# Kernel optimization log

Hardware: AMD Instinct MI355X
Metric: run time of the kernel (lower is better)

Reference implementation:

```python
import math
import jax, jax.numpy as jnp
import numpy as np

B, H, W, C = 16, 64, 64, 256


def setup_inputs() -> dict:
    key = jax.random.key(0)
    ks = jax.random.split(key, 6)
    return {
        "h": jax.random.normal(ks[0], (B, H, W, C), jnp.float32),
        # grouped 3x3 perception conv: groups=C, in/groups=1, out=3C
        "w_perc": jax.random.normal(ks[1], (3 * C, 1, 3, 3), jnp.float32) * 0.1,
        "b_perc": jnp.zeros((3 * C,), jnp.float32),
        # update_net: 1x1 conv 3C->2C, GELU, 1x1 conv 2C->C
        "w_up1": jax.random.normal(ks[2], (2 * C, 3 * C, 1, 1), jnp.float32) * 0.02,
        "b_up1": jnp.zeros((2 * C,), jnp.float32),
        "w_up2": jax.random.normal(ks[3], (C, 2 * C, 1, 1), jnp.float32) * 0.02,
        "b_up2": jnp.zeros((C,), jnp.float32),
        # lin_qkv: Linear C -> 3C (torch weight layout [out,in])
        "w_qkv": jax.random.normal(ks[4], (3 * C, C), jnp.float32) * 0.02,
        "b_qkv": jnp.zeros((3 * C,), jnp.float32),
    }


_POS = [(-1, -1), (-1, 0), (-1, 1), (0, -1), (0, 0), (0, 1), (1, -1), (1, 0), (1, 1)]


def _local_attn(hn, w_qkv, b_qkv):
    """3x3 windowed local attention (zero-padded borders), NHWC in/out."""
    Bb, Hh, Ww, Cc = hn.shape
    qkv = jnp.einsum('bhwc,dc->bhwd', hn, w_qkv) + b_qkv
    q, k, v = jnp.split(qkv, 3, axis=-1)
    kp = jnp.pad(k, ((0, 0), (1, 1), (1, 1), (0, 0)))
    vp = jnp.pad(v, ((0, 0), (1, 1), (1, 1), (0, 0)))
    scale = 1.0 / math.sqrt(Cc)
    # scores over the 9 neighbor offsets -> [B,H,W,9]
    scores = jnp.stack(
        [(q * kp[:, 1 + dy:1 + dy + Hh, 1 + dx:1 + dx + Ww, :]).sum(-1) for dy, dx in _POS],
        axis=-1) * scale
    w = jax.nn.softmax(scores, axis=-1)
    out = jnp.zeros_like(v)
    for i, (dy, dx) in enumerate(_POS):
        out = out + w[..., i:i + 1] * vp[:, 1 + dy:1 + dy + Hh, 1 + dx:1 + dx + Ww, :]
    return out


def reference(h, w_perc, b_perc, w_up1, b_up1, w_up2, b_up2, w_qkv, b_qkv):
    # eval-mode forward: noise / dropout / stochastic mask are identity
    Cc = h.shape[-1]
    x = jnp.transpose(h, (0, 3, 1, 2))  # NCHW
    perceived = jax.lax.conv_general_dilated(
        x, w_perc, window_strides=(1, 1), padding='SAME',
        feature_group_count=Cc,
        dimension_numbers=('NCHW', 'OIHW', 'NCHW')) + b_perc[None, :, None, None]
    hid = jnp.einsum('bphw,dp->bdhw', perceived, w_up1[:, :, 0, 0]) + b_up1[None, :, None, None]
    hid = jax.nn.gelu(hid, approximate=False)
    dx = jnp.einsum('bdhw,cd->bchw', hid, w_up2[:, :, 0, 0]) + b_up2[None, :, None, None]
    x_new = x + dx  # stochastic_update in eval mode
    h_new = jnp.transpose(x_new, (0, 2, 3, 1))  # NHWC
    h_attn = _local_attn(h_new, w_qkv, b_qkv)
    return h_new + h_attn
```

## Files before the change

kernel.cpp:

```cpp
#include <hip/hip_runtime.h>
#include <math.h>


typedef unsigned short u16;
typedef __bf16 bf16x8 __attribute__((ext_vector_type(8)));
typedef float floatx4 __attribute__((ext_vector_type(4)));

__device__ int g_flag;
__device__ __align__(16) u16 g_h[16777216];
__device__ __align__(16) u16 g_perc[50331648];
__device__ __align__(16) u16 g_hnew[16777216];
__device__ __align__(16) u16 g_wperc[6912];
__device__ __align__(16) u16 g_bperc[768];
__device__ __align__(16) u16 g_wup1[393216];
__device__ __align__(16) u16 g_bup1[512];
__device__ __align__(16) u16 g_wup2[131072];
__device__ __align__(16) u16 g_bup2[256];
__device__ __align__(16) u16 g_wqkv[196608];
__device__ __align__(16) u16 g_bqkv[768];

__device__ __forceinline__ float b2f(u16 x) {
  unsigned int u = ((unsigned int)x) << 16;
  float f;
  __builtin_memcpy(&f, &u, 4);
  return f;
}
__device__ __forceinline__ u16 f2b(float f) {
  unsigned int u;
  __builtin_memcpy(&u, &f, 4);
  u += 0x7FFFu + ((u >> 16) & 1u);
  return (u16)(u >> 16);
}
__device__ __forceinline__ void gload16(const u16* g, u16* l) {
  __builtin_amdgcn_global_load_lds(
      (const __attribute__((address_space(1))) unsigned int*)g,
      (__attribute__((address_space(3))) unsigned int*)l, 16, 0, 0);
}
__device__ __forceinline__ void up8(const uint4& v, float* f) {
  f[0] = b2f((u16)(v.x & 0xFFFF)); f[1] = b2f((u16)(v.x >> 16));
  f[2] = b2f((u16)(v.y & 0xFFFF)); f[3] = b2f((u16)(v.y >> 16));
  f[4] = b2f((u16)(v.z & 0xFFFF)); f[5] = b2f((u16)(v.z >> 16));
  f[6] = b2f((u16)(v.w & 0xFFFF)); f[7] = b2f((u16)(v.w >> 16));
}
__device__ __forceinline__ void ld8(const u16* p, float* f) {
  uint4 v = *(const uint4*)p;
  up8(v, f);
}

__global__ __launch_bounds__(256) void probe_kernel(const u16* __restrict__ h) {
  __shared__ int hit;
  if (threadIdx.x == 0) hit = 0;
  __syncthreads();
  int local = 0;
  for (int i = threadIdx.x; i < 8192; i += 256) {
    u16 v = h[2 * i];
    if ((v & 0x7F80) == 0x7F80) local = 1;
  }
  if (local) atomicOr(&hit, 1);
  __syncthreads();
  if (threadIdx.x == 0) g_flag = hit;
}

__global__ __launch_bounds__(256) void conv_w_kernel(
    const void* i1, const void* i2, const void* i3, const void* i4,
    const void* i5, const void* i6, const void* i7, const void* i8) {
  const void* srcs[8] = {i1, i2, i3, i4, i5, i6, i7, i8};
  u16* dsts[8] = {g_wperc, g_bperc, g_wup1, g_bup1,
                  g_wup2,  g_bup2,  g_wqkv, g_bqkv};
  const int szs[8] = {6912, 768, 393216, 512, 131072, 256, 196608, 768};
  const int fp32 = g_flag;
  const int stride = gridDim.x * 256;
  for (int gw = blockIdx.x * 256 + threadIdx.x; gw < 730112; gw += stride) {
    int seg = 0, off = gw;
    while (off >= szs[seg]) { off -= szs[seg]; ++seg; }
    dsts[seg][off] = fp32 ? f2b(((const float*)srcs[seg])[off])
                          : ((const u16*)srcs[seg])[off];
  }
}

__global__ __launch_bounds__(256) void perc_kernel(const void* __restrict__ hin) {
  __shared__ __align__(16) u16 sw[3456];
  __shared__ __align__(16) u16 sb[384];
  const int lb = (blockIdx.x & 7) * 256 + (blockIdx.x >> 3);
  const int bid = lb >> 1;
  const int chalf = lb & 1;
  const int b = bid >> 6, y = bid & 63;
  const int xi = threadIdx.x >> 6;
  const int cl = threadIdx.x & 63;
  const int c0 = chalf * 128 + cl * 2;
  for (int i = threadIdx.x; i < 3456; i += 256) sw[i] = g_wperc[chalf * 3456 + i];
  for (int i = threadIdx.x; i < 384; i += 256) sb[i] = g_bperc[chalf * 384 + i];
  const int fp32 = g_flag;
  __syncthreads();
  float w[2][27], bias[2][3];
#pragma unroll
  for (int ch = 0; ch < 2; ++ch) {
    const int lc = cl * 2 + ch;
#pragma unroll
    for (int t = 0; t < 3; ++t) {
      bias[ch][t] = b2f(sb[3 * lc + t]);
#pragma unroll
      for (int j = 0; j < 9; ++j)
        w[ch][t * 9 + j] = b2f(sw[(3 * lc + t) * 9 + j]);
    }
  }
  float hv[3][3][2];
  auto loadcol = [&](int xx, int cc) {
#pragma unroll
    for (int r = 0; r < 3; ++r) {
      const int yy = y - 1 + r;
      const bool ok = ((unsigned)yy < 64u) && ((unsigned)xx < 64u);
      if (ok) {
        const size_t idx = (((size_t)(b * 64 + yy) * 64) + xx) * 256 + c0;
        if (fp32) {
          const float2 v = *(const float2*)((const float*)hin + idx);
          hv[r][cc][0] = v.x;
          hv[r][cc][1] = v.y;
        } else {
          const unsigned v = *(const unsigned*)((const u16*)hin + idx);
          hv[r][cc][0] = b2f((u16)(v & 0xFFFF));
          hv[r][cc][1] = b2f((u16)(v >> 16));
        }
      } else {
        hv[r][cc][0] = 0.0f;
        hv[r][cc][1] = 0.0f;
      }
    }
  };
  const int x0 = xi * 16;
  loadcol(x0 - 1, 0);
  loadcol(x0, 1);
#pragma unroll
  for (int k = 0; k < 16; ++k) {
    const int x = x0 + k;
    loadcol(x + 1, (k + 2) % 3);
    const int cL = k % 3, cM = (k + 1) % 3, cR = (k + 2) % 3;
    const size_t pix = (size_t)(b * 64 + y) * 64 + x;
    *(unsigned*)&g_h[pix * 256 + c0] =
        (unsigned)f2b(hv[1][cM][0]) | ((unsigned)f2b(hv[1][cM][1]) << 16);
    u16* op = &g_perc[pix * 768 + 3 * c0];
    unsigned pk[3];
#pragma unroll
    for (int ch = 0; ch < 2; ++ch) {
#pragma unroll
      for (int t = 0; t < 3; ++t) {
        const float* wt = &w[ch][t * 9];
        float a = bias[ch][t];
        a += hv[0][cL][ch] * wt[0] + hv[0][cM][ch] * wt[1] + hv[0][cR][ch] * wt[2];
        a += hv[1][cL][ch] * wt[3] + hv[1][cM][ch] * wt[4] + hv[1][cR][ch] * wt[5];
        a += hv[2][cL][ch] * wt[6] + hv[2][cM][ch] * wt[7] + hv[2][cR][ch] * wt[8];
        const int o = 3 * ch + t;
        const unsigned bb = f2b(a);
        if (o & 1) pk[o >> 1] |= bb << 16; else pk[o >> 1] = bb;
      }
    }
    *(unsigned*)(op) = pk[0];
    *(unsigned*)(op + 2) = pk[1];
    *(unsigned*)(op + 4) = pk[2];
  }
}

__global__ __launch_bounds__(512, 2) void fused_mlp_qkv() {
  __shared__ __align__(16) u16 L[81920];
  const int tid = threadIdx.x;
  const int w = tid >> 6, lane = tid & 63;
  const int ln = lane & 15, quad = lane >> 4, lnx = ln & 7;
  const int wmi = w >> 2, wni = w & 3;
  const int m_blk = (blockIdx.x & 7) * 64 + (blockIdx.x >> 3);
  const int m0 = m_blk * 128;

  auto stageA = [&](int t) {
    u16* dst = &L[(t & 1) * 8192];
#pragma unroll
    for (int ld = 0; ld < 2; ++ld) {
      const int s = ld * 512 + tid;
      const int sr = s >> 3, sc = (s & 7) ^ (sr & 7);
      gload16(&g_perc[(size_t)(m0 + sr) * 768 + t * 64 + sc * 8], dst + s * 8);
    }
  };
  auto stageB1 = [&](int t) {
    u16* dst = &L[16384 + (t & 1) * 32768];
#pragma unroll
    for (int ld = 0; ld < 8; ++ld) {
      const int s = ld * 512 + tid;
      const int sr = s >> 3, sc = (s & 7) ^ (sr & 7);
      gload16(&g_wup1[(size_t)sr * 768 + t * 64 + sc * 8], dst + s * 8);
    }
  };

  floatx4 acc[4][8] = {};
  stageA(0); stageB1(0);
  for (int u = 0; u < 12; ++u) {
    asm volatile("s_waitcnt vmcnt(0)" ::: "memory");
    __builtin_amdgcn_s_barrier();
    if (u + 1 < 12) { stageA(u + 1); stageB1(u + 1); }
    const u16* Ab = &L[(u & 1) * 8192];
    const u16* Bb = &L[16384 + (u & 1) * 32768];
    bf16x8 a[4][2];
#pragma unroll
    for (int i = 0; i < 4; ++i) {
      const int row = wmi * 64 + i * 16 + ln;
#pragma unroll
      for (int ks = 0; ks < 2; ++ks)
        a[i][ks] = *(const bf16x8*)(Ab + (row * 8 + ((ks * 4 + quad) ^ lnx)) * 8);
    }
    __builtin_amdgcn_s_setprio(1);
#pragma unroll
    for (int jg = 0; jg < 2; ++jg) {
      bf16x8 b[4][2];
#pragma unroll
      for (int jj = 0; jj < 4; ++jj) {
        const int row = wni * 128 + (jg * 4 + jj) * 16 + ln;
#pragma unroll
        for (int ks = 0; ks < 2; ++ks)
          b[jj][ks] =
              *(const bf16x8*)(Bb + (row * 8 + ((ks * 4 + quad) ^ lnx)) * 8);
      }
#pragma unroll
      for (int i = 0; i < 4; ++i)
#pragma unroll
        for (int jj = 0; jj < 4; ++jj)
#pragma unroll
          for (int ks = 0; ks < 2; ++ks)
            acc[i][jg * 4 + jj] = __builtin_amdgcn_mfma_f32_16x16x32_bf16(
                a[i][ks], b[jj][ks], acc[i][jg * 4 + jj], 0, 0, 0);
    }
    __builtin_amdgcn_s_setprio(0);
  }
  __builtin_amdgcn_s_barrier();
#pragma unroll
  for (int i = 0; i < 4; ++i) {
#pragma unroll
    for (int j = 0; j < 8; ++j) {
      const int n = wni * 128 + j * 16 + ln;
      const float bv = b2f(g_bup1[n]);
      const int ch = n >> 3;
#pragma unroll
      for (int rr = 0; rr < 4; ++rr) {
        const int r = wmi * 64 + i * 16 + quad * 4 + rr;
        float v = acc[i][j][rr] + bv;
        v = 0.5f * v * (1.0f + erff(v * 0.70710678118654752f));
        L[((size_t)r * 64 + ((ch & 56) | ((ch & 7) ^ (r & 7)))) * 8 + (n & 7)] =
            f2b(v);
      }
    }
  }
  asm volatile("s_waitcnt lgkmcnt(0)" ::: "memory");
  __builtin_amdgcn_s_barrier();

  auto stageW2 = [&](int t) {
    u16* dst = &L[65536 + (t & 1) * 8192];
#pragma unroll
    for (int ld = 0; ld < 2; ++ld) {
      const int s = ld * 512 + tid;
      const int sr = s >> 2, sc = (s & 3) ^ (sr & 3);
      gload16(&g_wup2[(size_t)sr * 512 + t * 32 + sc * 8], dst + s * 8);
    }
  };
  floatx4 acB[4][4] = {};
  stageW2(0);
  for (int t = 0; t < 16; ++t) {
    asm volatile("s_waitcnt vmcnt(0)" ::: "memory");
    __builtin_amdgcn_s_barrier();
    if (t + 1 < 16) stageW2(t + 1);
    const u16* Wb = &L[65536 + (t & 1) * 8192];
    const int kt = t >> 1, ks = t & 1;
    bf16x8 a[4], b[4];
#pragma unroll
    for (int i = 0; i < 4; ++i) {
      const int row = wmi * 64 + i * 16 + ln;
      a[i] = *(const bf16x8*)(
          &L[((size_t)row * 64 + kt * 8 + ((ks * 4 + quad) ^ (row & 7))) * 8]);
    }
#pragma unroll
    for (int j = 0; j < 4; ++j) {
      const int row = wni * 64 + j * 16 + ln;
      b[j] = *(const bf16x8*)(Wb + (row * 4 + (quad ^ (row & 3))) * 8);
    }
    __builtin_amdgcn_s_setprio(1);
#pragma unroll
    for (int i = 0; i < 4; ++i)
#pragma unroll
      for (int j = 0; j < 4; ++j)
        acB[i][j] = __builtin_amdgcn_mfma_f32_16x16x32_bf16(a[i], b[j],
                                                            acB[i][j], 0, 0, 0);
    __builtin_amdgcn_s_setprio(0);
  }
  __builtin_amdgcn_s_barrier();
#pragma unroll
  for (int i = 0; i < 4; ++i) {
#pragma unroll
    for (int j = 0; j < 4; ++j) {
      const int n = wni * 64 + j * 16 + ln;
      const float bv = b2f(g_bup2[n]);
      const int ch = n >> 3;
#pragma unroll
      for (int rr = 0; rr < 4; ++rr) {
        const int r = wmi * 64 + i * 16 + quad * 4 + rr;
        float v = acB[i][j][rr] + bv;
        v += b2f(g_h[(size_t)(m0 + r) * 256 + n]);
        const u16 bb = f2b(v);
        g_hnew[(size_t)(m0 + r) * 256 + n] = bb;
        L[((size_t)r * 32 + ((ch & 24) | ((ch & 7) ^ (r & 7)))) * 8 + (n & 7)] =
            bb;
      }
    }
  }
  auto stageWq = [&](int tt) {
    u16* dst = &L[32768 + (tt % 3) * 16384];
    const int c = tt >> 2, t = tt & 3;
#pragma unroll
    for (int ld = 0; ld < 4; ++ld) {
      const int s = ld * 512 + tid;
      const int sr = s >> 3, sc = (s & 7) ^ (sr & 7);
      gload16(&g_wqkv[(size_t)(c * 256 + sr) * 256 + t * 64 + sc * 8],
              dst + s * 8);
    }
  };
  stageWq(0);
  stageWq(1);
  asm volatile("s_waitcnt lgkmcnt(0)" ::: "memory");
  __builtin_amdgcn_s_barrier();
  for (int c = 0; c < 3; ++c) {
    floatx4 acC[4][4] = {};
    for (int t = 0; t < 4; ++t) {
      const int tt = c * 4 + t;
      if (tt < 11) asm volatile("s_waitcnt vmcnt(4)" ::: "memory");
      else         asm volatile("s_waitcnt vmcnt(0)" ::: "memory");
      __builtin_amdgcn_s_barrier();
      if (tt + 2 < 12) stageWq(tt + 2);
      const u16* Wb = &L[32768 + (tt % 3) * 16384];
      bf16x8 a[4][2], b[4][2];
#pragma unroll
      for (int i = 0; i < 4; ++i) {
        const int row = wmi * 64 + i * 16 + ln;
#pragma unroll
        for (int ks = 0; ks < 2; ++ks)
          a[i][ks] = *(const bf16x8*)(
              &L[((size_t)row * 32 + t * 8 + ((ks * 4 + quad) ^ (row & 7))) *
                 8]);
      }
#pragma unroll
      for (int j = 0; j < 4; ++j) {
        const int row = wni * 64 + j * 16 + ln;
#pragma unroll
        for (int ks = 0; ks < 2; ++ks)
          b[j][ks] =
              *(const bf16x8*)(Wb + (row * 8 + ((ks * 4 + quad) ^ lnx)) * 8);
      }
      __builtin_amdgcn_s_setprio(1);
#pragma unroll
      for (int i = 0; i < 4; ++i)
#pragma unroll
        for (int j = 0; j < 4; ++j)
#pragma unroll
          for (int ks = 0; ks < 2; ++ks)
            acC[i][j] = __builtin_amdgcn_mfma_f32_16x16x32_bf16(
                a[i][ks], b[j][ks], acC[i][j], 0, 0, 0);
      __builtin_amdgcn_s_setprio(0);
    }
#pragma unroll
    for (int i = 0; i < 4; ++i) {
#pragma unroll
      for (int j = 0; j < 4; ++j) {
        const int n = wni * 64 + j * 16 + ln;
        const float bv = b2f(g_bqkv[c * 256 + n]);
#pragma unroll
        for (int rr = 0; rr < 4; ++rr) {
          const int r = wmi * 64 + i * 16 + quad * 4 + rr;
          g_perc[(size_t)(m0 + r) * 768 + c * 256 + n] = f2b(acC[i][j][rr] + bv);
        }
      }
    }
  }
}

__global__ __launch_bounds__(256) void attn_kernel(void* __restrict__ outv) {
  const int wv = threadIdx.x >> 6, lane = threadIdx.x & 63;
  const int half = lane >> 5, cl = lane & 31;
  const int c0 = cl * 8;
  const int lb = (blockIdx.x & 7) * 128 + (blockIdx.x >> 3);
  const int run = lb * 8 + wv * 2 + half;
  const int row = run >> 3;
  const int y = row & 63;
  const int x0 = (run & 7) * 8;
  const int fp32 = g_flag;

  uint4 Kw[3][3], Vw[3][3], tK[3], tV[3];
  auto fetch = [&](int xx, uint4 (&K3)[3], uint4 (&V3)[3]) {
#pragma unroll
    for (int r = 0; r < 3; ++r) {
      const int yy = y - 1 + r;
      if (((unsigned)yy < 64u) && ((unsigned)xx < 64u)) {
        const size_t np = (size_t)(row - 1 + r) * 64 + xx;
        K3[r] = *(const uint4*)(g_perc + np * 768 + 256 + c0);
        V3[r] = *(const uint4*)(g_perc + np * 768 + 512 + c0);
      } else {
        K3[r] = make_uint4(0, 0, 0, 0);
        V3[r] = make_uint4(0, 0, 0, 0);
      }
    }
  };
  fetch(x0 - 1, tK, tV);
#pragma unroll
  for (int r = 0; r < 3; ++r) { Kw[r][0] = tK[r]; Vw[r][0] = tV[r]; }
  fetch(x0, tK, tV);
#pragma unroll
  for (int r = 0; r < 3; ++r) { Kw[r][1] = tK[r]; Vw[r][1] = tV[r]; }
  fetch(x0 + 1, tK, tV);

#pragma unroll
  for (int k = 0; k < 8; ++k) {
    const int x = x0 + k;
    const int sR = (k + 2) % 3;
#pragma unroll
    for (int r = 0; r < 3; ++r) { Kw[r][sR] = tK[r]; Vw[r][sR] = tV[r]; }
    fetch(x + 2, tK, tV);

    const size_t pix = (size_t)row * 64 + x;
    float q[8];
    ld8(g_perc + pix * 768 + c0, q);
    float a[8];
    ld8(g_hnew + pix * 256 + c0, a);

    float s[9];
#pragma unroll
    for (int j = 0; j < 9; ++j) {
      float kv[8];
      up8(Kw[j / 3][(k + j % 3) % 3], kv);
      float p = q[0] * kv[0] + q[1] * kv[1] + q[2] * kv[2] + q[3] * kv[3] +
                q[4] * kv[4] + q[5] * kv[5] + q[6] * kv[6] + q[7] * kv[7];
#pragma unroll
      for (int off = 16; off >= 1; off >>= 1) p += __shfl_xor(p, off, 64);
      s[j] = p * 0.0625f;
    }
    float mx = s[0];
#pragma unroll
    for (int j = 1; j < 9; ++j) mx = fmaxf(mx, s[j]);
    float e[9], den = 0.0f;
#pragma unroll
    for (int j = 0; j < 9; ++j) {
      e[j] = expf(s[j] - mx);
      den += e[j];
    }
    const float inv = 1.0f / den;
#pragma unroll
    for (int j = 0; j < 9; ++j) {
      const float wgt = e[j] * inv;
      float vv[8];
      up8(Vw[j / 3][(k + j % 3) % 3], vv);
#pragma unroll
      for (int t = 0; t < 8; ++t) a[t] += wgt * vv[t];
    }
    const size_t o = pix * 256 + c0;
    if (fp32) {
      float4 r0 = {a[0], a[1], a[2], a[3]};
      float4 r1 = {a[4], a[5], a[6], a[7]};
      *(float4*)((float*)outv + o) = r0;
      *(float4*)((float*)outv + o + 4) = r1;
    } else {
      uint4 r;
      r.x = (unsigned)f2b(a[0]) | ((unsigned)f2b(a[1]) << 16);
      r.y = (unsigned)f2b(a[2]) | ((unsigned)f2b(a[3]) << 16);
      r.z = (unsigned)f2b(a[4]) | ((unsigned)f2b(a[5]) << 16);
      r.w = (unsigned)f2b(a[6]) | ((unsigned)f2b(a[7]) << 16);
      *(uint4*)((u16*)outv + o) = r;
    }
  }
}

extern "C" void kernel_launch(void* const* d_in, const int* in_sizes, int n_in,
                              void* d_out, int d_out_size, void* d_ws,
                              size_t ws_size, hipStream_t stream) {
  (void)d_ws; (void)ws_size;
  probe_kernel<<<1, 256, 0, stream>>>((const u16*)d_in[0]);
  conv_w_kernel<<<360, 256, 0, stream>>>(d_in[1], d_in[2], d_in[3], d_in[4],
                                         d_in[5], d_in[6], d_in[7], d_in[8]);
  perc_kernel<<<2048, 256, 0, stream>>>(d_in[0]);
  fused_mlp_qkv<<<512, 512, 0, stream>>>();
  attn_kernel<<<1024, 256, 0, stream>>>(d_out);
}
```

Before: 381.6 us.

## Deepen first GEMM pipeline to four stages with smaller K tiles and new swizzle

The first GEMM of the fused MLP kernel drops from a double-buffered 64-wide K tile to a quad-buffered 32-wide K tile with three tiles in flight. It uses partial vmcnt waits so the global loads of later stages overlap with the MFMA work on the current one. The LDS swizzle changes to an XOR on (row>>1)&3, also applied to the W2 staging, to reduce bank conflicts for 4-chunk rows. The cost is twice as many barriers per K, with less MFMA work between them, and the hand-counted vmcnt values have to match the number of loads issued per stage.

```diff
diff --git a/kernel.cpp b/kernel.cpp
--- a/kernel.cpp
+++ b/kernel.cpp
@@ -169,61 +169,54 @@
   const int m_blk = (blockIdx.x & 7) * 64 + (blockIdx.x >> 3);
   const int m0 = m_blk * 128;
 
-  auto stageA = [&](int t) {
-    u16* dst = &L[(t & 1) * 8192];
-#pragma unroll
-    for (int ld = 0; ld < 2; ++ld) {
+  auto stageAW = [&](int t) {
+    u16* base = &L[(t & 3) * 20480];
+    {
+      const int s = tid;
+      const int sr = s >> 2, sc = (s & 3) ^ ((sr >> 1) & 3);
+      gload16(&g_perc[(size_t)(m0 + sr) * 768 + t * 32 + sc * 8], base + s * 8);
+    }
+    u16* wb = base + 4096;
+#pragma unroll
+    for (int ld = 0; ld < 4; ++ld) {
       const int s = ld * 512 + tid;
-      const int sr = s >> 3, sc = (s & 7) ^ (sr & 7);
-      gload16(&g_perc[(size_t)(m0 + sr) * 768 + t * 64 + sc * 8], dst + s * 8);
+      const int sr = s >> 2, sc = (s & 3) ^ ((sr >> 1) & 3);
+      gload16(&g_wup1[(size_t)sr * 768 + t * 32 + sc * 8], wb + s * 8);
     }
   };
-  auto stageB1 = [&](int t) {
-    u16* dst = &L[16384 + (t & 1) * 32768];
-#pragma unroll
-    for (int ld = 0; ld < 8; ++ld) {
-      const int s = ld * 512 + tid;
-      const int sr = s >> 3, sc = (s & 7) ^ (sr & 7);
-      gload16(&g_wup1[(size_t)sr * 768 + t * 64 + sc * 8], dst + s * 8);
-    }
-  };
 
   floatx4 acc[4][8] = {};
-  stageA(0); stageB1(0);
-  for (int u = 0; u < 12; ++u) {
-    asm volatile("s_waitcnt vmcnt(0)" ::: "memory");
+  stageAW(0); stageAW(1); stageAW(2);
+  for (int u = 0; u < 24; ++u) {
+    if (u < 22)       asm volatile("s_waitcnt vmcnt(10)" ::: "memory");
+    else if (u == 22) asm volatile("s_waitcnt vmcnt(5)" ::: "memory");
+    else              asm volatile("s_waitcnt vmcnt(0)" ::: "memory");
     __builtin_amdgcn_s_barrier();
-    if (u + 1 < 12) { stageA(u + 1); stageB1(u + 1); }
-    const u16* Ab = &L[(u & 1) * 8192];
-    const u16* Bb = &L[16384 + (u & 1) * 32768];
-    bf16x8 a[4][2];
+    if (u + 3 < 24) stageAW(u + 3);
+    const u16* Ab = &L[(u & 3) * 20480];
+    const u16* Bb = Ab + 4096;
+    bf16x8 a[4];
 #pragma unroll
     for (int i = 0; i < 4; ++i) {
       const int row = wmi * 64 + i * 16 + ln;
-#pragma unroll
-      for (int ks = 0; ks < 2; ++ks)
-        a[i][ks] = *(const bf16x8*)(Ab + (row * 8 + ((ks * 4 + quad) ^ lnx)) * 8);
+      a[i] = *(const bf16x8*)(Ab + (row * 4 + (quad ^ ((row >> 1) & 3))) * 8);
     }
     __builtin_amdgcn_s_setprio(1);
 #pragma unroll
     for (int jg = 0; jg < 2; ++jg) {
-      bf16x8 b[4][2];
+      bf16x8 b[4];
 #pragma unroll
       for (int jj = 0; jj < 4; ++jj) {
         const int row = wni * 128 + (jg * 4 + jj) * 16 + ln;
-#pragma unroll
-        for (int ks = 0; ks < 2; ++ks)
-          b[jj][ks] =
-              *(const bf16x8*)(Bb + (row * 8 + ((ks * 4 + quad) ^ lnx)) * 8);
+        b[jj] =
+            *(const bf16x8*)(Bb + (row * 4 + (quad ^ ((row >> 1) & 3))) * 8);
       }
 #pragma unroll
       for (int i = 0; i < 4; ++i)
 #pragma unroll
         for (int jj = 0; jj < 4; ++jj)
-#pragma unroll
-          for (int ks = 0; ks < 2; ++ks)
-            acc[i][jg * 4 + jj] = __builtin_amdgcn_mfma_f32_16x16x32_bf16(
-                a[i][ks], b[jj][ks], acc[i][jg * 4 + jj], 0, 0, 0);
+          acc[i][jg * 4 + jj] = __builtin_amdgcn_mfma_f32_16x16x32_bf16(
+              a[i], b[jj], acc[i][jg * 4 + jj], 0, 0, 0);
     }
     __builtin_amdgcn_s_setprio(0);
   }
@@ -253,7 +246,7 @@
 #pragma unroll
     for (int ld = 0; ld < 2; ++ld) {
       const int s = ld * 512 + tid;
-      const int sr = s >> 2, sc = (s & 3) ^ (sr & 3);
+      const int sr = s >> 2, sc = (s & 3) ^ ((sr >> 1) & 3);
       gload16(&g_wup2[(size_t)sr * 512 + t * 32 + sc * 8], dst + s * 8);
     }
   };
@@ -275,7 +268,7 @@
 #pragma unroll
     for (int j = 0; j < 4; ++j) {
       const int row = wni * 64 + j * 16 + ln;
-      b[j] = *(const bf16x8*)(Wb + (row * 4 + (quad ^ (row & 3))) * 8);
+      b[j] = *(const bf16x8*)(Wb + (row * 4 + (quad ^ ((row >> 1) & 3))) * 8);
     }
     __builtin_amdgcn_s_setprio(1);
 #pragma unroll
```

Result: no change. 386.9 us (+1.4%).
